# Performance work log

Hardware: AMD Instinct MI355X
Metric: run time of the kernel (lower is better)

## Reference

```python
import jax, jax.numpy as jnp
import numpy as np

N = 50000      # nodes
E = 600000     # edges
D = 128        # in_channels
H = 128        # hidden_channels
C = 16         # out_channels
L = 3          # num GIN layers
G = 512        # graphs in batch
BN_EPS = 1e-5


def setup_inputs() -> dict:
    key = jax.random.key(0)
    ks = jax.random.split(key, 18)
    s = 0.05
    x = jax.random.normal(ks[0], (N, D), jnp.float32)
    edge_index = jax.random.randint(ks[1], (2, E), 0, N, dtype=jnp.int32)
    batch = jnp.sort(jax.random.randint(ks[2], (N,), 0, G, dtype=jnp.int32))
    # per-layer GIN MLP params (in_channels == hidden, so layers stack uniformly)
    W1s = jax.random.normal(ks[3], (L, D, H), jnp.float32) * s
    b1s = jnp.zeros((L, H), jnp.float32)
    g1s = jnp.ones((L, H), jnp.float32)    # inner BatchNorm gamma
    be1s = jnp.zeros((L, H), jnp.float32)  # inner BatchNorm beta
    W2s = jax.random.normal(ks[4], (L, H, H), jnp.float32) * s
    b2s = jnp.zeros((L, H), jnp.float32)
    gns = jnp.ones((L, H), jnp.float32)    # outer (post-conv) BatchNorm gamma
    bns = jnp.zeros((L, H), jnp.float32)
    # classifier head
    Wc1 = jax.random.normal(ks[5], (H, H), jnp.float32) * s
    bc1 = jnp.zeros((H,), jnp.float32)
    gc = jnp.ones((H,), jnp.float32)
    bec = jnp.zeros((H,), jnp.float32)
    Wc2 = jax.random.normal(ks[6], (H, C), jnp.float32) * s
    bc2 = jnp.zeros((C,), jnp.float32)
    return dict(x=x, edge_index=edge_index, batch=batch, W1s=W1s, b1s=b1s,
                g1s=g1s, be1s=be1s, W2s=W2s, b2s=b2s, gns=gns, bns=bns,
                Wc1=Wc1, bc1=bc1, gc=gc, bec=bec, Wc2=Wc2, bc2=bc2)


def _bn(h, gamma, beta):
    # BatchNorm1d in training mode: batch statistics over the node/row dim
    m = jnp.mean(h, axis=0)
    v = jnp.mean((h - m) ** 2, axis=0)
    return gamma * (h - m) * jax.lax.rsqrt(v + BN_EPS) + beta


def reference(x, edge_index, batch, W1s, b1s, g1s, be1s, W2s, b2s, gns, bns,
              Wc1, bc1, gc, bec, Wc2, bc2):
    src, dst = edge_index[0], edge_index[1]
    h = x
    for l in range(L):
        # GINConv, eps=0: mlp((1+eps)*x_i + sum_{j->i} x_j)
        agg = jax.ops.segment_sum(h[src], dst, num_segments=N) + h
        z = agg @ W1s[l] + b1s[l]
        z = jax.nn.relu(_bn(z, g1s[l], be1s[l]))
        z = z @ W2s[l] + b2s[l]
        h = jax.nn.relu(_bn(z, gns[l], bns[l]))
    # global mean pool over graphs
    counts = jax.ops.segment_sum(jnp.ones((N,), h.dtype), batch, num_segments=G)
    pooled = jax.ops.segment_sum(h, batch, num_segments=G) / jnp.maximum(counts, 1.0)[:, None]
    z = pooled @ Wc1 + bc1
    z = jax.nn.relu(_bn(z, gc, bec))
    return z @ Wc2 + bc2  # [G, C]
```

## Files before the change

### kernel.cpp

```cpp
#include <hip/hip_runtime.h>
#include <hip/hip_fp16.h>

#define NN 50000
#define NE 600000
#define DIM 128
#define NG 512
#define OC 16
#define BN_EPS 1e-5f

typedef __attribute__((ext_vector_type(8))) short short8v;
typedef __attribute__((ext_vector_type(4))) float f32x4;

__device__ inline unsigned short f2bf(float f) {
    unsigned u = __float_as_uint(f);
    u = u + 0x7FFF + ((u >> 16) & 1);
    return (unsigned short)(u >> 16);
}
__device__ inline float bf2f(unsigned short h) {
    return __uint_as_float(((unsigned)h) << 16);
}
__device__ inline float hbits2f(short s) {
    __half_raw hr; hr.x = (unsigned short)s;
    return __half2float(__half(hr));
}
__device__ inline short f2hbits(float f) {
    __half h = __float2half(f);
    short r;
    __builtin_memcpy(&r, &h, 2);
    return r;
}

__global__ void k_hist(const int* __restrict__ dst, int* __restrict__ deg, int e) {
    int i = blockIdx.x * blockDim.x + threadIdx.x;
    if (i < e) atomicAdd(&deg[dst[i]], 1);
}

__global__ void k_scan1(const int* __restrict__ deg, int* __restrict__ pre,
                        int* __restrict__ bsum, int n) {
    __shared__ int lds[1024];
    int t = threadIdx.x;
    int i = blockIdx.x * 1024 + t;
    int v = (i < n) ? deg[i] : 0;
    lds[t] = v;
    __syncthreads();
#pragma unroll
    for (int off = 1; off < 1024; off <<= 1) {
        int add = (t >= off) ? lds[t - off] : 0;
        __syncthreads();
        lds[t] += add;
        __syncthreads();
    }
    if (i < n) pre[i] = lds[t] - v;
    if (t == 1023) bsum[blockIdx.x] = lds[1023];
}

__global__ void k_scan2(int* __restrict__ bsum, int nb) {
    int t = threadIdx.x;
    int v = (t < nb) ? bsum[t] : 0;
    int orig = v;
#pragma unroll
    for (int off = 1; off < 64; off <<= 1) {
        int u = __shfl_up(v, off);
        if (t >= off) v += u;
    }
    if (t < nb) bsum[t] = v - orig;
}

__global__ void k_scan3(const int* __restrict__ pre, const int* __restrict__ bsum,
                        int* __restrict__ row_start, int* __restrict__ cursor, int n) {
    int i = blockIdx.x * blockDim.x + threadIdx.x;
    if (i < n) {
        int r = pre[i] + bsum[i >> 10];
        row_start[i] = r;
        cursor[i] = r;
    }
    if (i == 0) row_start[n] = NE;
}

__global__ void k_scatter(const int* __restrict__ src, const int* __restrict__ dst,
                          int* __restrict__ cursor, int* __restrict__ col, int e) {
    int i = blockIdx.x * blockDim.x + threadIdx.x;
    if (i < e) {
        int d = dst[i];
        int p = atomicAdd(&cursor[d], 1);
        col[p] = src[i];
    }
}

__global__ void k_gstart(const int* __restrict__ batch, int* __restrict__ gstart, int n) {
    int i = blockIdx.x * blockDim.x + threadIdx.x;
    if (i >= n) return;
    int b = batch[i];
    int bp = (i == 0) ? -1 : batch[i - 1];
    for (int g = bp + 1; g <= b; g++) gstart[g] = i;
    if (i == n - 1) {
        for (int g = b + 1; g <= NG; g++) gstart[g] = n;
    }
}

__global__ void k_transform0(const float* __restrict__ in, __half* __restrict__ out, int n4) {
    int i = blockIdx.x * blockDim.x + threadIdx.x;
    if (i >= n4) return;
    float4 v = ((const float4*)in)[i];
    __half2 o0 = __floats2half2_rn(v.x, v.y);
    __half2 o1 = __floats2half2_rn(v.z, v.w);
    uint2 pk;
    pk.x = *(unsigned*)&o0;
    pk.y = *(unsigned*)&o1;
    ((uint2*)out)[i] = pk;
}

template <int TRANSFORM>
__global__ void k_aggregate_q(const __half* __restrict__ Ht, const int* __restrict__ rs,
                              const int* __restrict__ col,
                              const float* __restrict__ stats, const float* __restrict__ gamma,
                              const float* __restrict__ beta, float invn,
                              __half* __restrict__ out, int n) {
    __shared__ float sst[256];
    int tid = threadIdx.x;
    if (TRANSFORM && tid < 128) {
        float s = stats[tid], q = stats[128 + tid];
        float m = s * invn;
        float var = fmaxf(q * invn - m * m, 0.f);
        float r = rsqrtf(var + BN_EPS);
        float sc = gamma[tid] * r;
        sst[tid] = sc;
        sst[128 + tid] = beta[tid] - m * sc;
    }
    if (TRANSFORM) __syncthreads();

    int node = blockIdx.x * 16 + (tid >> 4);
    if (node >= n) return;
    int ql = tid & 15;
    int c = ql * 8;
    float sc[8], sh[8];
    if (TRANSFORM) {
#pragma unroll
        for (int j = 0; j < 8; j++) { sc[j] = sst[c + j]; sh[j] = sst[128 + c + j]; }
    }

    const short8v* Hp = (const short8v*)Ht;
    float acc[8];
    short8v hv = Hp[(size_t)node * 16 + ql];
#pragma unroll
    for (int j = 0; j < 8; j++) {
        float f = hbits2f(hv[j]);
        if (TRANSFORM) f = fmaxf(fmaf(f, sc[j], sh[j]), 0.f);
        acc[j] = f;
    }
    int s = rs[node], e = rs[node + 1];
    int i = s;
    for (; i + 1 < e; i += 2) {
        int j0 = col[i], j1 = col[i + 1];
        short8v u0 = Hp[(size_t)j0 * 16 + ql];
        short8v u1 = Hp[(size_t)j1 * 16 + ql];
#pragma unroll
        for (int j = 0; j < 8; j++) {
            float f0 = hbits2f(u0[j]);
            float f1 = hbits2f(u1[j]);
            if (TRANSFORM) {
                f0 = fmaxf(fmaf(f0, sc[j], sh[j]), 0.f);
                f1 = fmaxf(fmaf(f1, sc[j], sh[j]), 0.f);
            }
            acc[j] += f0 + f1;
        }
    }
    if (i < e) {
        short8v u0 = Hp[(size_t)col[i] * 16 + ql];
#pragma unroll
        for (int j = 0; j < 8; j++) {
            float f0 = hbits2f(u0[j]);
            if (TRANSFORM) f0 = fmaxf(fmaf(f0, sc[j], sh[j]), 0.f);
            acc[j] += f0;
        }
    }
    short8v o;
#pragma unroll
    for (int j = 0; j < 8; j++) o[j] = f2hbits(acc[j]);
    ((short8v*)out)[(size_t)node * 16 + ql] = o;
}

__global__ void k_prepw(const float* __restrict__ W1s, const float* __restrict__ W2s,
                        const float* __restrict__ Wc1, unsigned short* __restrict__ wfrag) {
    int idx = blockIdx.x * blockDim.x + threadIdx.x;
    if (idx >= 7 * 8 * 4 * 64) return;
    int lane = idx & 63;
    int k0 = (idx >> 6) & 3;
    int ct = (idx >> 8) & 7;
    int m = idx >> 11;
    const float* Wsrc = (m < 3) ? (W1s + (size_t)m * 16384)
                      : (m < 6) ? (W2s + (size_t)(m - 3) * 16384)
                                : Wc1;
    int colc = ct * 16 + (lane & 15);
    int kbase = k0 * 32 + (lane >> 4) * 8;
    short8v hi, lo;
#pragma unroll
    for (int j = 0; j < 8; j++) {
        float w = Wsrc[(size_t)(kbase + j) * 128 + colc];
        unsigned short h = f2bf(w);
        hi[j] = (short)h;
        lo[j] = (short)f2bf(w - bf2f(h));
    }
    size_t fo = ((size_t)(ct * 4 + k0) * 64 + lane) * 8;
    *(short8v*)(wfrag + (size_t)(m * 2 + 0) * 16384 + fo) = hi;
    *(short8v*)(wfrag + (size_t)(m * 2 + 1) * 16384 + fo) = lo;
}

#define MFMA(A8, B8, C4) __builtin_amdgcn_mfma_f32_16x16x32_bf16(A8, B8, C4, 0, 0, 0)

#define STORE_STATS(ACT, ACC0, ACC1, SUB)                                          \
    if (ACT) {                                                                     \
        int rowb = (SUB) * 16 + kb * 4;                                            \
        _Pragma("unroll")                                                          \
        for (int j = 0; j < 4; j++) {                                              \
            size_t i0 = (size_t)(rowb + j) * 128 + ct0 * 16 + rlo;                 \
            size_t i1 = (size_t)(rowb + j) * 128 + ct1 * 16 + rlo;                 \
            if (ZHALF) {                                                           \
                ((__half*)Zout)[i0] = __float2half(ACC0[j]);                       \
                ((__half*)Zout)[i1] = __float2half(ACC1[j]);                       \
            } else {                                                               \
                ((float*)Zout)[i0] = ACC0[j];                                      \
                ((float*)Zout)[i1] = ACC1[j];                                      \
            }                                                                      \
        }                                                                          \
        float s0 = ACC0[0] + ACC0[1] + ACC0[2] + ACC0[3];                          \
        float q0 = ACC0[0]*ACC0[0] + ACC0[1]*ACC0[1] + ACC0[2]*ACC0[2] + ACC0[3]*ACC0[3]; \
        float s1 = ACC1[0] + ACC1[1] + ACC1[2] + ACC1[3];                          \
        float q1 = ACC1[0]*ACC1[0] + ACC1[1]*ACC1[1] + ACC1[2]*ACC1[2] + ACC1[3]*ACC1[3]; \
        s0 += __shfl_xor(s0, 16); s0 += __shfl_xor(s0, 32);                        \
        q0 += __shfl_xor(q0, 16); q0 += __shfl_xor(q0, 32);                        \
        s1 += __shfl_xor(s1, 16); s1 += __shfl_xor(s1, 32);                        \
        q1 += __shfl_xor(q1, 16); q1 += __shfl_xor(q1, 32);                        \
        if (kb == 0) {                                                             \
            atomicAdd(&sred[ct0 * 16 + rlo], s0);                                  \
            atomicAdd(&sred[128 + ct0 * 16 + rlo], q0);                            \
            atomicAdd(&sred[ct1 * 16 + rlo], s1);                                  \
            atomicAdd(&sred[128 + ct1 * 16 + rlo], q1);                            \
        }                                                                          \
    }

template <int TRANSFORM, int ZHALF>
__global__ __launch_bounds__(256) void k_gemm_mfma(
        const __half* __restrict__ A, const unsigned short* __restrict__ wfragm,
        const float* __restrict__ bias,
        const float* __restrict__ statsIn, const float* __restrict__ gamma,
        const float* __restrict__ beta, float invn,
        void* __restrict__ Zout, float* __restrict__ statsOut, int nsub) {
    __shared__ short8v wldsHi[1024];
    __shared__ short8v wldsLo[1024];
    __shared__ float sred[256];
    __shared__ float sst[256];
    int tid = threadIdx.x;
    int wid = tid >> 6, lane = tid & 63;
    int sub0 = (blockIdx.x * 4 + wid) * 2;
    bool act0 = sub0 < nsub, act1 = sub0 + 1 < nsub;
    int rlo = lane & 15, kb = lane >> 4;

    sred[tid] = 0.f;
    if (TRANSFORM && tid < 128) {
        float s = statsIn[tid], q = statsIn[128 + tid];
        float m = s * invn;
        float var = fmaxf(q * invn - m * m, 0.f);
        float rs = rsqrtf(var + BN_EPS);
        float sc = gamma[tid] * rs;
        sst[tid] = sc;
        sst[128 + tid] = beta[tid] - m * sc;
    }
    __syncthreads();

    short8v ahi[2][4], alo[2][4];
#pragma unroll
    for (int ss = 0; ss < 2; ss++) {
        bool act = ss ? act1 : act0;
        if (act) {
            const __half* ap = A + ((size_t)(sub0 + ss) * 16 + rlo) * 128;
#pragma unroll
            for (int k0 = 0; k0 < 4; k0++) {
                int c = k0 * 32 + kb * 8;
                short8v hv = *(const short8v*)(ap + c);
#pragma unroll
                for (int j = 0; j < 8; j++) {
                    float f = hbits2f(hv[j]);
                    if (TRANSFORM) f = fmaxf(fmaf(f, sst[c + j], sst[128 + c + j]), 0.f);
                    unsigned short hb = f2bf(f);
                    ahi[ss][k0][j] = (short)hb;
                    alo[ss][k0][j] = (short)f2bf(f - bf2f(hb));
                }
            }
        } else {
#pragma unroll
            for (int k0 = 0; k0 < 4; k0++) {
                ahi[ss][k0] = short8v{0,0,0,0,0,0,0,0};
                alo[ss][k0] = short8v{0,0,0,0,0,0,0,0};
            }
        }
    }

    const float4* wsrc = (const float4*)wfragm;
    float4* dH = (float4*)wldsHi;
    float4* dL = (float4*)wldsLo;

#pragma unroll
    for (int p = 0; p < 2; p++) {
        if (p) __syncthreads();
#pragma unroll
        for (int i = 0; i < 4; i++) {
            dH[tid + 256 * i] = wsrc[p * 1024 + tid + 256 * i];
            dL[tid + 256 * i] = wsrc[2048 + p * 1024 + tid + 256 * i];
        }
        __syncthreads();
#pragma unroll
        for (int cc = 0; cc < 2; cc++) {
            int ctp = 2 * p + cc;
            int ct0 = ctp * 2, ct1 = ct0 + 1;
            int l0 = ct0 - 4 * p, l1 = ct1 - 4 * p;
            float bb0 = bias[ct0 * 16 + rlo], bb1 = bias[ct1 * 16 + rlo];
            f32x4 acc00 = {bb0, bb0, bb0, bb0};
            f32x4 acc01 = {bb1, bb1, bb1, bb1};
            f32x4 acc10 = {bb0, bb0, bb0, bb0};
            f32x4 acc11 = {bb1, bb1, bb1, bb1};
#pragma unroll
            for (int k0 = 0; k0 < 4; k0++) {
                short8v bh0 = wldsHi[(l0 * 4 + k0) * 64 + lane];
                short8v bh1 = wldsHi[(l1 * 4 + k0) * 64 + lane];
                short8v bl0 = wldsLo[(l0 * 4 + k0) * 64 + lane];
                short8v bl1 = wldsLo[(l1 * 4 + k0) * 64 + lane];
                acc00 = MFMA(ahi[0][k0], bh0, acc00);
                acc10 = MFMA(ahi[1][k0], bh0, acc10);
                acc01 = MFMA(ahi[0][k0], bh1, acc01);
                acc11 = MFMA(ahi[1][k0], bh1, acc11);
                acc00 = MFMA(alo[0][k0], bh0, acc00);
                acc10 = MFMA(alo[1][k0], bh0, acc10);
                acc01 = MFMA(alo[0][k0], bh1, acc01);
                acc11 = MFMA(alo[1][k0], bh1, acc11);
                acc00 = MFMA(ahi[0][k0], bl0, acc00);
                acc10 = MFMA(ahi[1][k0], bl0, acc10);
                acc01 = MFMA(ahi[0][k0], bl1, acc01);
                acc11 = MFMA(ahi[1][k0], bl1, acc11);
            }
            STORE_STATS(act0, acc00, acc01, sub0);
            STORE_STATS(act1, acc10, acc11, sub0 + 1);
        }
    }
    __syncthreads();
    if (tid < 128) {
        atomicAdd(&statsOut[tid], sred[tid]);
        atomicAdd(&statsOut[128 + tid], sred[128 + tid]);
    }
}

__global__ void k_pool_seg(const __half* __restrict__ H, const int* __restrict__ gstart,
                           const float* __restrict__ stats, const float* __restrict__ gamma,
                           const float* __restrict__ beta, float invn,
                           __half* __restrict__ out) {
    int g = blockIdx.x;
    int s = gstart[g], e = gstart[g + 1];
    int t = threadIdx.x;
    int lane = t & 63, wave = t >> 6;
    int c0 = lane * 2;
    float sc0, sc1, sh0, sh1;
    {
        float s0 = stats[c0], q0 = stats[128 + c0];
        float m0 = s0 * invn;
        float r0 = rsqrtf(fmaxf(q0 * invn - m0 * m0, 0.f) + BN_EPS);
        sc0 = gamma[c0] * r0; sh0 = beta[c0] - m0 * sc0;
        float s1 = stats[c0 + 1], q1 = stats[129 + c0];
        float m1 = s1 * invn;
        float r1 = rsqrtf(fmaxf(q1 * invn - m1 * m1, 0.f) + BN_EPS);
        sc1 = gamma[c0 + 1] * r1; sh1 = beta[c0 + 1] - m1 * sc1;
    }
    const __half2* Hp = (const __half2*)H;
    float ax = 0.f, ay = 0.f;
    for (int r = s + wave; r < e; r += 4) {
        float2 v = __half22float2(Hp[(size_t)r * 64 + lane]);
        ax += fmaxf(fmaf(v.x, sc0, sh0), 0.f);
        ay += fmaxf(fmaf(v.y, sc1, sh1), 0.f);
    }
    __shared__ float red[2][256];
    red[0][t] = ax;
    red[1][t] = ay;
    __syncthreads();
    if (wave == 0) {
        float inv = 1.f / fmaxf((float)(e - s), 1.f);
        float sx = red[0][lane] + red[0][64 + lane] + red[0][128 + lane] + red[0][192 + lane];
        float sy = red[1][lane] + red[1][64 + lane] + red[1][128 + lane] + red[1][192 + lane];
        ((__half2*)out)[g * 64 + lane] = __floats2half2_rn(sx * inv, sy * inv);
    }
}

__global__ void k_final(const float* __restrict__ Zh, const float* __restrict__ stats,
                        const float* __restrict__ gamma, const float* __restrict__ beta,
                        float invn, const float* __restrict__ Wc2,
                        const float* __restrict__ bc2, float* __restrict__ out) {
    __shared__ float Wl[128 * 16];
    __shared__ float Al[32 * 128];
    int tid = threadIdx.x;
    int kc = tid & 127;
    float s = stats[kc], q = stats[128 + kc];
    float m = s * invn;
    float rs = rsqrtf(fmaxf(q * invn - m * m, 0.f) + BN_EPS);
    float sck = gamma[kc] * rs;
    float shk = beta[kc] - m * sck;
#pragma unroll
    for (int i = 0; i < 4; i++) Wl[tid + 512 * i] = Wc2[tid + 512 * i];
#pragma unroll
    for (int i = 0; i < 8; i++) {
        int idx = tid + 512 * i;
        int gl = idx >> 7, k = idx & 127;
        float a = Zh[(size_t)(blockIdx.x * 32 + gl) * 128 + k];
        Al[idx] = fmaxf(fmaf(a, sck, shk), 0.f);
    }
    __syncthreads();
    int g = tid >> 4, c = tid & 15;
    float acc = bc2[c];
#pragma unroll 8
    for (int k = 0; k < 128; k++) acc = fmaf(Al[g * 128 + k], Wl[k * 16 + c], acc);
    out[(size_t)(blockIdx.x * 32 + g) * 16 + c] = acc;
}

extern "C" void kernel_launch(void* const* d_in, const int* in_sizes, int n_in,
                              void* d_out, int out_size, void* d_ws, size_t ws_size,
                              hipStream_t stream) {
    (void)in_sizes; (void)n_in; (void)out_size; (void)ws_size;
    const float* x    = (const float*)d_in[0];
    const int*   ei   = (const int*)d_in[1];
    const int*   srcv = ei;
    const int*   dstv = ei + NE;
    const int*   batch = (const int*)d_in[2];
    const float* W1s = (const float*)d_in[3];
    const float* b1s = (const float*)d_in[4];
    const float* g1s = (const float*)d_in[5];
    const float* be1s = (const float*)d_in[6];
    const float* W2s = (const float*)d_in[7];
    const float* b2s = (const float*)d_in[8];
    const float* gns = (const float*)d_in[9];
    const float* bns = (const float*)d_in[10];
    const float* Wc1 = (const float*)d_in[11];
    const float* bc1 = (const float*)d_in[12];
    const float* gc  = (const float*)d_in[13];
    const float* bec = (const float*)d_in[14];
    const float* Wc2 = (const float*)d_in[15];
    const float* bc2 = (const float*)d_in[16];
    float* out = (float*)d_out;

    char* ws = (char*)d_ws;
    size_t off = 0;
    auto alloc = [&](size_t bytes) -> char* {
        char* p = ws + off;
        off += (bytes + 255) & ~(size_t)255;
        return p;
    };
    int*   deg     = (int*)alloc(50048 * 4);
    float* statsZ  = (float*)alloc(7 * 256 * 4);
    size_t zeroBytes = off;
    int*   row_start = (int*)alloc((NN + 64) * 4);
    int*   cursor    = (int*)alloc((NN + 64) * 4);
    int*   pre       = (int*)alloc((NN + 64) * 4);
    int*   bsum      = (int*)alloc(64 * 4);
    int*   col       = (int*)alloc((NE + 64) * 4);
    int*   gstart    = (int*)alloc((NG + 1) * 4);
    unsigned short* wfrag = (unsigned short*)alloc((size_t)7 * 2 * 16384 * 2);
    __half* Ht     = (__half*)alloc((size_t)NN * 128 * 2);
    __half* aggH   = (__half*)alloc((size_t)NN * 128 * 2);
    __half* bufBh  = (__half*)alloc((size_t)NN * 128 * 2);
    __half* bufCh  = (__half*)alloc((size_t)NN * 128 * 2);
    __half* headAh = (__half*)alloc((size_t)NG * 128 * 2);
    float*  bufF   = (float*)alloc((size_t)NG * 128 * 4);

    hipMemsetAsync(d_ws, 0, zeroBytes, stream);

    k_prepw<<<56, 256, 0, stream>>>(W1s, W2s, Wc1, wfrag);

    k_hist<<<(NE + 255) / 256, 256, 0, stream>>>(dstv, deg, NE);
    int nb = (NN + 1023) / 1024;
    k_scan1<<<nb, 1024, 0, stream>>>(deg, pre, bsum, NN);
    k_scan2<<<1, 64, 0, stream>>>(bsum, nb);
    k_scan3<<<(NN + 255) / 256, 256, 0, stream>>>(pre, bsum, row_start, cursor, NN);
    k_scatter<<<(NE + 255) / 256, 256, 0, stream>>>(srcv, dstv, cursor, col, NE);
    k_gstart<<<(NN + 255) / 256, 256, 0, stream>>>(batch, gstart, NN);

    int n4 = NN * 32;
    int tGrid = (n4 + 255) / 256;
    int aggGrid = NN / 16;
    int nsub = NN / 16;
    int gGrid = (nsub + 7) / 8;
    float invN = 1.f / NN;

    k_transform0<<<tGrid, 256, 0, stream>>>(x, Ht, n4);

    for (int l = 0; l < 3; l++) {
        float* s1 = statsZ + (size_t)(2 * l) * 256;
        float* s2 = statsZ + (size_t)(2 * l + 1) * 256;
        if (l == 0)
            k_aggregate_q<0><<<aggGrid, 256, 0, stream>>>(
                Ht, row_start, col, nullptr, nullptr, nullptr, 0.f, aggH, NN);
        else
            k_aggregate_q<1><<<aggGrid, 256, 0, stream>>>(
                bufCh, row_start, col, statsZ + (size_t)(2 * l - 1) * 256,
                gns + (l - 1) * 128, bns + (l - 1) * 128, invN, aggH, NN);
        k_gemm_mfma<0, 1><<<gGrid, 256, 0, stream>>>(
            aggH, wfrag + (size_t)(2 * l) * 16384, b1s + l * 128,
            nullptr, nullptr, nullptr, 0.f, bufBh, s1, nsub);
        k_gemm_mfma<1, 1><<<gGrid, 256, 0, stream>>>(
            bufBh, wfrag + (size_t)(2 * (3 + l)) * 16384, b2s + l * 128,
            s1, g1s + l * 128, be1s + l * 128, invN, bufCh, s2, nsub);
    }

    float* s2last = statsZ + (size_t)5 * 256;
    float* sHead  = statsZ + (size_t)6 * 256;
    k_pool_seg<<<NG, 256, 0, stream>>>(bufCh, gstart, s2last, gns + 2 * 128,
                                       bns + 2 * 128, invN, headAh);
    k_gemm_mfma<0, 0><<<4, 256, 0, stream>>>(
        headAh, wfrag + (size_t)12 * 16384, bc1,
        nullptr, nullptr, nullptr, 0.f, bufF, sHead, NG / 16);
    k_final<<<16, 512, 0, stream>>>(bufF, sHead, gc, bec, 1.f / NG, Wc2, bc2, out);
}
```

Baseline: 341.3 us.

## Switch GEMMs to fp16 MFMA, merge scan kernels, unroll gather by four

The split-bf16 three-pass MFMA scheme becomes an fp16 scheme: activations already stored as fp16 feed the MFMA directly, and only the weights keep a hi/lo split, so each tile needs two MFMA passes instead of three and skips the per-element bf16 conversion. The block-sum scan is folded into the third scan kernel, which removes one launch. The aggregation gather loop is unrolled to four neighbors to keep more loads in flight. Activations now get fp16 precision only, with no residual term, which may cost some accuracy.

Result: faster. 310.9 us (-8.9%).

```diff
diff --git a/kernel.cpp b/kernel.cpp
--- a/kernel.cpp
+++ b/kernel.cpp
@@ -9,16 +9,9 @@
 #define BN_EPS 1e-5f
 
 typedef __attribute__((ext_vector_type(8))) short short8v;
+typedef __attribute__((ext_vector_type(8))) _Float16 half8v;
 typedef __attribute__((ext_vector_type(4))) float f32x4;
 
-__device__ inline unsigned short f2bf(float f) {
-    unsigned u = __float_as_uint(f);
-    u = u + 0x7FFF + ((u >> 16) & 1);
-    return (unsigned short)(u >> 16);
-}
-__device__ inline float bf2f(unsigned short h) {
-    return __uint_as_float(((unsigned)h) << 16);
-}
 __device__ inline float hbits2f(short s) {
     __half_raw hr; hr.x = (unsigned short)s;
     return __half2float(__half(hr));
@@ -28,6 +21,11 @@
     short r;
     __builtin_memcpy(&r, &h, 2);
     return r;
+}
+__device__ inline half8v s2h8(short8v s) {
+    half8v h;
+    __builtin_memcpy(&h, &s, 16);
+    return h;
 }
 
 __global__ void k_hist(const int* __restrict__ dst, int* __restrict__ deg, int e) {
@@ -54,23 +52,25 @@
     if (t == 1023) bsum[blockIdx.x] = lds[1023];
 }
 
-__global__ void k_scan2(int* __restrict__ bsum, int nb) {
+__global__ void k_scan3(const int* __restrict__ pre, const int* __restrict__ bsum,
+                        int* __restrict__ row_start, int* __restrict__ cursor,
+                        int n, int nb) {
+    __shared__ int boff[64];
     int t = threadIdx.x;
-    int v = (t < nb) ? bsum[t] : 0;
-    int orig = v;
-#pragma unroll
-    for (int off = 1; off < 64; off <<= 1) {
-        int u = __shfl_up(v, off);
-        if (t >= off) v += u;
-    }
-    if (t < nb) bsum[t] = v - orig;
-}
-
-__global__ void k_scan3(const int* __restrict__ pre, const int* __restrict__ bsum,
-                        int* __restrict__ row_start, int* __restrict__ cursor, int n) {
-    int i = blockIdx.x * blockDim.x + threadIdx.x;
+    if (t < 64) {
+        int v = (t < nb) ? bsum[t] : 0;
+        int orig = v;
+#pragma unroll
+        for (int off = 1; off < 64; off <<= 1) {
+            int u = __shfl_up(v, off);
+            if (t >= off) v += u;
+        }
+        boff[t] = v - orig;
+    }
+    __syncthreads();
+    int i = blockIdx.x * blockDim.x + t;
     if (i < n) {
-        int r = pre[i] + bsum[i >> 10];
+        int r = pre[i] + boff[i >> 10];
         row_start[i] = r;
         cursor[i] = r;
     }
@@ -140,40 +140,32 @@
     }
 
     const short8v* Hp = (const short8v*)Ht;
+#define TRF(F) (TRANSFORM ? fmaxf(fmaf((F), sc[j], sh[j]), 0.f) : (F))
     float acc[8];
     short8v hv = Hp[(size_t)node * 16 + ql];
 #pragma unroll
-    for (int j = 0; j < 8; j++) {
-        float f = hbits2f(hv[j]);
-        if (TRANSFORM) f = fmaxf(fmaf(f, sc[j], sh[j]), 0.f);
-        acc[j] = f;
-    }
+    for (int j = 0; j < 8; j++) { float f = hbits2f(hv[j]); acc[j] = TRF(f); }
     int s = rs[node], e = rs[node + 1];
     int i = s;
-    for (; i + 1 < e; i += 2) {
-        int j0 = col[i], j1 = col[i + 1];
+    for (; i + 3 < e; i += 4) {
+        int j0 = col[i], j1 = col[i + 1], j2 = col[i + 2], j3 = col[i + 3];
         short8v u0 = Hp[(size_t)j0 * 16 + ql];
         short8v u1 = Hp[(size_t)j1 * 16 + ql];
+        short8v u2 = Hp[(size_t)j2 * 16 + ql];
+        short8v u3 = Hp[(size_t)j3 * 16 + ql];
 #pragma unroll
         for (int j = 0; j < 8; j++) {
-            float f0 = hbits2f(u0[j]);
-            float f1 = hbits2f(u1[j]);
-            if (TRANSFORM) {
-                f0 = fmaxf(fmaf(f0, sc[j], sh[j]), 0.f);
-                f1 = fmaxf(fmaf(f1, sc[j], sh[j]), 0.f);
-            }
-            acc[j] += f0 + f1;
+            float f0 = hbits2f(u0[j]), f1 = hbits2f(u1[j]);
+            float f2 = hbits2f(u2[j]), f3 = hbits2f(u3[j]);
+            acc[j] += TRF(f0) + TRF(f1) + TRF(f2) + TRF(f3);
         }
     }
-    if (i < e) {
+    for (; i < e; i++) {
         short8v u0 = Hp[(size_t)col[i] * 16 + ql];
 #pragma unroll
-        for (int j = 0; j < 8; j++) {
-            float f0 = hbits2f(u0[j]);
-            if (TRANSFORM) f0 = fmaxf(fmaf(f0, sc[j], sh[j]), 0.f);
-            acc[j] += f0;
-        }
-    }
+        for (int j = 0; j < 8; j++) { float f0 = hbits2f(u0[j]); acc[j] += TRF(f0); }
+    }
+#undef TRF
     short8v o;
 #pragma unroll
     for (int j = 0; j < 8; j++) o[j] = f2hbits(acc[j]);
@@ -197,16 +189,16 @@
 #pragma unroll
     for (int j = 0; j < 8; j++) {
         float w = Wsrc[(size_t)(kbase + j) * 128 + colc];
-        unsigned short h = f2bf(w);
-        hi[j] = (short)h;
-        lo[j] = (short)f2bf(w - bf2f(h));
+        short hb = f2hbits(w);
+        hi[j] = hb;
+        lo[j] = f2hbits(w - hbits2f(hb));
     }
     size_t fo = ((size_t)(ct * 4 + k0) * 64 + lane) * 8;
     *(short8v*)(wfrag + (size_t)(m * 2 + 0) * 16384 + fo) = hi;
     *(short8v*)(wfrag + (size_t)(m * 2 + 1) * 16384 + fo) = lo;
 }
 
-#define MFMA(A8, B8, C4) __builtin_amdgcn_mfma_f32_16x16x32_bf16(A8, B8, C4, 0, 0, 0)
+#define MFMA16(A8, B8, C4) __builtin_amdgcn_mfma_f32_16x16x32_f16(A8, B8, C4, 0, 0, 0)
 
 #define STORE_STATS(ACT, ACC0, ACC1, SUB)                                          \
     if (ACT) {                                                                     \
@@ -268,7 +260,7 @@
     }
     __syncthreads();
 
-    short8v ahi[2][4], alo[2][4];
+    half8v af[2][4];
 #pragma unroll
     for (int ss = 0; ss < 2; ss++) {
         bool act = ss ? act1 : act0;
@@ -278,21 +270,19 @@
             for (int k0 = 0; k0 < 4; k0++) {
                 int c = k0 * 32 + kb * 8;
                 short8v hv = *(const short8v*)(ap + c);
-#pragma unroll
-                for (int j = 0; j < 8; j++) {
-                    float f = hbits2f(hv[j]);
-                    if (TRANSFORM) f = fmaxf(fmaf(f, sst[c + j], sst[128 + c + j]), 0.f);
-                    unsigned short hb = f2bf(f);
-                    ahi[ss][k0][j] = (short)hb;
-                    alo[ss][k0][j] = (short)f2bf(f - bf2f(hb));
+                if (TRANSFORM) {
+#pragma unroll
+                    for (int j = 0; j < 8; j++) {
+                        float f = hbits2f(hv[j]);
+                        f = fmaxf(fmaf(f, sst[c + j], sst[128 + c + j]), 0.f);
+                        hv[j] = f2hbits(f);
+                    }
                 }
+                af[ss][k0] = s2h8(hv);
             }
         } else {
 #pragma unroll
-            for (int k0 = 0; k0 < 4; k0++) {
-                ahi[ss][k0] = short8v{0,0,0,0,0,0,0,0};
-                alo[ss][k0] = short8v{0,0,0,0,0,0,0,0};
-            }
+            for (int k0 = 0; k0 < 4; k0++) af[ss][k0] = half8v{0,0,0,0,0,0,0,0};
         }
     }
 
@@ -321,22 +311,18 @@
             f32x4 acc11 = {bb1, bb1, bb1, bb1};
 #pragma unroll
             for (int k0 = 0; k0 < 4; k0++) {
-                short8v bh0 = wldsHi[(l0 * 4 + k0) * 64 + lane];
-                short8v bh1 = wldsHi[(l1 * 4 + k0) * 64 + lane];
-                short8v bl0 = wldsLo[(l0 * 4 + k0) * 64 + lane];
-                short8v bl1 = wldsLo[(l1 * 4 + k0) * 64 + lane];
-                acc00 = MFMA(ahi[0][k0], bh0, acc00);
-                acc10 = MFMA(ahi[1][k0], bh0, acc10);
-                acc01 = MFMA(ahi[0][k0], bh1, acc01);
-                acc11 = MFMA(ahi[1][k0], bh1, acc11);
-                acc00 = MFMA(alo[0][k0], bh0, acc00);
-                acc10 = MFMA(alo[1][k0], bh0, acc10);
-                acc01 = MFMA(alo[0][k0], bh1, acc01);
-                acc11 = MFMA(alo[1][k0], bh1, acc11);
-                acc00 = MFMA(ahi[0][k0], bl0, acc00);
-                acc10 = MFMA(ahi[1][k0], bl0, acc10);
-                acc01 = MFMA(ahi[0][k0], bl1, acc01);
-                acc11 = MFMA(ahi[1][k0], bl1, acc11);
+                half8v bh0 = s2h8(wldsHi[(l0 * 4 + k0) * 64 + lane]);
+                half8v bh1 = s2h8(wldsHi[(l1 * 4 + k0) * 64 + lane]);
+                half8v bl0 = s2h8(wldsLo[(l0 * 4 + k0) * 64 + lane]);
+                half8v bl1 = s2h8(wldsLo[(l1 * 4 + k0) * 64 + lane]);
+                acc00 = MFMA16(af[0][k0], bh0, acc00);
+                acc10 = MFMA16(af[1][k0], bh0, acc10);
+                acc01 = MFMA16(af[0][k0], bh1, acc01);
+                acc11 = MFMA16(af[1][k0], bh1, acc11);
+                acc00 = MFMA16(af[0][k0], bl0, acc00);
+                acc10 = MFMA16(af[1][k0], bl0, acc10);
+                acc01 = MFMA16(af[0][k0], bl1, acc01);
+                acc11 = MFMA16(af[1][k0], bl1, acc11);
             }
             STORE_STATS(act0, acc00, acc01, sub0);
             STORE_STATS(act1, acc10, acc11, sub0 + 1);
@@ -474,8 +460,7 @@
     k_hist<<<(NE + 255) / 256, 256, 0, stream>>>(dstv, deg, NE);
     int nb = (NN + 1023) / 1024;
     k_scan1<<<nb, 1024, 0, stream>>>(deg, pre, bsum, NN);
-    k_scan2<<<1, 64, 0, stream>>>(bsum, nb);
-    k_scan3<<<(NN + 255) / 256, 256, 0, stream>>>(pre, bsum, row_start, cursor, NN);
+    k_scan3<<<(NN + 255) / 256, 256, 0, stream>>>(pre, bsum, row_start, cursor, NN, nb);
     k_scatter<<<(NE + 255) / 256, 256, 0, stream>>>(srcv, dstv, cursor, col, NE);
     k_gstart<<<(NN + 255) / 256, 256, 0, stream>>>(batch, gstart, NN);
 
```
